# Optimization experiments

Hardware: AMD Instinct MI355X
Metric: run time of the kernel (lower is better)

Reference implementation:

```python
import jax, jax.numpy as jnp
import numpy as np

B, T, D = 512, 512, 256          # batch, timesteps, input feature dim
H0, H1, H2, H3 = 32, 64, 64, 64  # VanillaRNN, LSTM, LSTM, GRU hidden sizes
NC = 12                          # num_cumulants


def setup_inputs() -> dict:
    key = jax.random.key(0)
    ks = jax.random.split(key, 12)
    f32 = jnp.float32

    def w(k, shape, fan_in):
        return jax.random.normal(k, shape, f32) * f32(1.0 / np.sqrt(fan_in))

    inp = {}
    inp["pixels_observation"] = jax.random.normal(ks[0], (B, T, D), f32)
    # VanillaRNN(32): input_to_hidden Linear(D->32), hidden_to_hidden Linear(32->32), both with bias
    inp["van_wi"] = w(ks[1], (D, H0), D)
    inp["van_bi"] = jnp.zeros((H0,), f32)
    inp["van_wh"] = w(ks[2], (H0, H0), H0)
    inp["van_bh"] = jnp.zeros((H0,), f32)
    # LSTM(64) on 32-dim input: Linear(32+64 -> 4*64)
    inp["lstm1_w"] = w(ks[3], (H0 + H1, 4 * H1), H0 + H1)
    inp["lstm1_b"] = jnp.zeros((4 * H1,), f32)
    # LSTM(64) on 64-dim input
    inp["lstm2_w"] = w(ks[4], (H1 + H2, 4 * H2), H1 + H2)
    inp["lstm2_b"] = jnp.zeros((4 * H2,), f32)
    # GRU(64)
    inp["gru_wi"] = w(ks[5], (H2, 3 * H3), H2)
    inp["gru_wh"] = w(ks[6], (H3, 3 * H3), H3)
    inp["gru_b"] = jnp.zeros((3 * H3,), f32)
    # MLP (32, 32, 12)
    inp["mlp_w1"] = w(ks[7], (H3, 32), H3)
    inp["mlp_b1"] = jnp.zeros((32,), f32)
    inp["mlp_w2"] = w(ks[8], (32, 32), 32)
    inp["mlp_b2"] = jnp.zeros((32,), f32)
    inp["mlp_w3"] = w(ks[9], (32, NC), 32)
    inp["mlp_b3"] = jnp.zeros((NC,), f32)
    # learned successor_features parameter (preference_vectors = ones(NC,1) constant)
    inp["successor_features"] = jax.random.normal(ks[10], (NC, 1), f32)
    inp["action_index"] = 0
    return inp


def _lstm_step(x, h, c, w, b):
    # haiku LSTM: gates on concat([x, h]); split order i, g, f, o; forget bias +1
    gated = jnp.concatenate([x, h], axis=-1) @ w + b
    i, g, f, o = jnp.split(gated, 4, axis=-1)
    c = jax.nn.sigmoid(f + 1.0) * c + jax.nn.sigmoid(i) * jnp.tanh(g)
    h = jax.nn.sigmoid(o) * jnp.tanh(c)
    return h, c


def reference(pixels_observation, van_wi, van_bi, van_wh, van_bh,
              lstm1_w, lstm1_b, lstm2_w, lstm2_b,
              gru_wi, gru_wh, gru_b,
              mlp_w1, mlp_b1, mlp_w2, mlp_b2, mlp_w3, mlp_b3,
              successor_features, action_index):
    assert action_index == 0  # source selects branch with a static Python int
    x = pixels_observation
    Bsz = x.shape[0]
    f32 = x.dtype

    def step(carry, x_t):
        h0, h1, c1, h2, c2, h3 = carry
        # VanillaRNN: relu(Wi x + bi + Wh h + bh)
        h0 = jax.nn.relu(x_t @ van_wi + van_bi + h0 @ van_wh + van_bh)
        h1, c1 = _lstm_step(h0, h1, c1, lstm1_w, lstm1_b)
        h2, c2 = _lstm_step(h1, h2, c2, lstm2_w, lstm2_b)
        # haiku GRU
        gates_x = h2 @ gru_wi                       # [B, 3H]
        zr_x, a_x = gates_x[:, :2 * H3], gates_x[:, 2 * H3:]
        zr = zr_x + h3 @ gru_wh[:, :2 * H3] + gru_b[:2 * H3]
        z, r = jnp.split(jax.nn.sigmoid(zr), 2, axis=-1)
        a = jnp.tanh(a_x + (r * h3) @ gru_wh[:, 2 * H3:] + gru_b[2 * H3:])
        h3 = (1.0 - z) * h3 + z * a
        return (h0, h1, c1, h2, c2, h3), None

    init = (jnp.zeros((Bsz, H0), f32),
            jnp.zeros((Bsz, H1), f32), jnp.zeros((Bsz, H1), f32),
            jnp.zeros((Bsz, H2), f32), jnp.zeros((Bsz, H2), f32),
            jnp.zeros((Bsz, H3), f32))
    carry, _ = jax.lax.scan(step, init, jnp.swapaxes(x, 0, 1))  # time-major scan
    emb = carry[-1]  # final GRU output = DeepRNN output at last timestep

    # MLP (32, 32, NC): relu on hidden layers, linear final layer
    emb = jax.nn.relu(emb @ mlp_w1 + mlp_b1)
    emb = jax.nn.relu(emb @ mlp_w2 + mlp_b2)
    emb = emb @ mlp_w3 + mlp_b3                     # [B, NC]

    preference_vectors = jnp.ones((NC, 1), f32)
    # einsum('ca,bc->ba', pref * succ, emb)
    policy_params = emb @ (preference_vectors * successor_features)  # [B, 1]
    return successor_features, preference_vectors, policy_params
```

## Files before the change

kernel.cpp:

```cpp
#include <hip/hip_runtime.h>
#include <stdint.h>

#define Tsz 512
#define Dsz 256
#define NINT 260

union UHp { uint32_t u; _Float16 s[2]; };
__device__ __forceinline__ uint32_t packh(float a, float b) {
    UHp x; x.s[0] = (_Float16)a; x.s[1] = (_Float16)b; return x.u;
}
__device__ __forceinline__ float dot2(uint32_t w, uint32_t a, float c) {
#if __has_builtin(__builtin_amdgcn_fdot2)
    typedef _Float16 h2 __attribute__((ext_vector_type(2)));
    union U { uint32_t u; h2 h; };
    U W, A; W.u = w; A.u = a;
    return __builtin_amdgcn_fdot2(W.h, A.h, c, false);
#else
    float d;
    asm("v_dot2_f32_f16 %0, %1, %2, %3" : "=v"(d) : "v"(w), "v"(a), "v"(c));
    return d;
#endif
}
__device__ __forceinline__ float fsig(float x)  { return 1.0f / (1.0f + __expf(-x)); }
__device__ __forceinline__ float ftanh(float x) { return 2.0f / (1.0f + __expf(-2.0f * x)) - 1.0f; }

__device__ __forceinline__ void barrier_lds() {
    asm volatile("s_waitcnt lgkmcnt(0)" ::: "memory");
    __builtin_amdgcn_s_barrier();
}

#define D4(ACC, WP, V) \
    do { ACC = dot2((WP)[0], (V).x, ACC); ACC = dot2((WP)[1], (V).y, ACC); \
         ACC = dot2((WP)[2], (V).z, ACC); ACC = dot2((WP)[3], (V).w, ACC); } while (0)
#define D4X(A, X, WP, V) \
    do { A = dot2((WP)[0], (V).x, A); X = dot2((WP)[1], (V).y, X); \
         A = dot2((WP)[2], (V).z, A); X = dot2((WP)[3], (V).w, X); } while (0)

__global__ __launch_bounds__(512, 1) void rnn_pipe5(
    const float* __restrict__ pix,
    const float* __restrict__ van_wi, const float* __restrict__ van_bi,
    const float* __restrict__ van_wh, const float* __restrict__ van_bh,
    const float* __restrict__ w1g, const float* __restrict__ b1g,
    const float* __restrict__ w2g, const float* __restrict__ b2g,
    const float* __restrict__ gwi, const float* __restrict__ gwh,
    const float* __restrict__ gb,
    const float* __restrict__ mw1, const float* __restrict__ mb1,
    const float* __restrict__ mw2, const float* __restrict__ mb2,
    const float* __restrict__ mw3, const float* __restrict__ mb3,
    const float* __restrict__ sf,
    float* __restrict__ out)
{
    const int tid  = threadIdx.x;
    const int wv   = tid >> 6;
    const int lane = tid & 63;
    const int r0   = 2 * blockIdx.x;

    __shared__ __align__(16) _Float16 xb [4][2][256];
    __shared__ __align__(16) _Float16 h0b[4][2][32];
    __shared__ __align__(16) _Float16 h1b[4][2][64];
    __shared__ __align__(16) _Float16 h2b[4][2][64];
    __shared__ __align__(16) _Float16 gxb[4][2][192];
    __shared__ __align__(16) _Float16 h3s[2][64];
    __shared__ __align__(16) _Float16 rh3s[2][64];
    __shared__ int flg[4];
    __shared__ float sHf[2][64];
    __shared__ float sT[2][64];
    __shared__ float sP[2][12];

    uint32_t wreg[128];
    float bz0 = 0.f, bz1 = 0.f, bz2 = 0.f;
    float st0 = 0.f, st1 = 0.f;
    float4 pxS[4];
    const float* pr0 = nullptr; const float* pr1 = nullptr;

    if (wv == 0) {
        const int c = lane & 31, s = lane >> 5;
#pragma unroll
        for (int j = 0; j < 64; ++j)
            wreg[j] = packh(van_wi[(128 * s + 2 * j) * 32 + c],
                            van_wi[(128 * s + 2 * j + 1) * 32 + c]);
#pragma unroll
        for (int j = 0; j < 8; ++j)
            wreg[64 + j] = packh(van_wh[(16 * s + 2 * j) * 32 + c],
                                 van_wh[(16 * s + 2 * j + 1) * 32 + c]);
        bz0 = van_bi[c] + van_bh[c];
        pr0 = pix + (size_t)r0 * Tsz * Dsz;
        pr1 = pr0 + (size_t)Tsz * Dsz;
#pragma unroll
        for (int t = 0; t < 2; ++t) {
            float4 p0 = *(const float4*)(pr0 + (size_t)t * Dsz + 4 * lane);
            float4 p1 = *(const float4*)(pr1 + (size_t)t * Dsz + 4 * lane);
            uint32_t* x0 = (uint32_t*)xb[t][0];
            uint32_t* x1 = (uint32_t*)xb[t][1];
            x0[2 * lane] = packh(p0.x, p0.y); x0[2 * lane + 1] = packh(p0.z, p0.w);
            x1[2 * lane] = packh(p1.x, p1.y); x1[2 * lane + 1] = packh(p1.z, p1.w);
        }
        pxS[0] = *(const float4*)(pr0 + 2 * (size_t)Dsz + 4 * lane);
        pxS[1] = *(const float4*)(pr1 + 2 * (size_t)Dsz + 4 * lane);
        pxS[2] = *(const float4*)(pr0 + 3 * (size_t)Dsz + 4 * lane);
        pxS[3] = *(const float4*)(pr1 + 3 * (size_t)Dsz + 4 * lane);
    } else if (wv <= 2) {
        const int p = tid - 64, u = p >> 1, odd = p & 1;
        const int c0 = odd ? 128 + u : u, c1 = c0 + 64;
#pragma unroll
        for (int j = 0; j < 48; ++j)
            wreg[j] = packh(w1g[(2 * j) * 256 + c0], w1g[(2 * j + 1) * 256 + c0]);
#pragma unroll
        for (int j = 0; j < 48; ++j)
            wreg[48 + j] = packh(w1g[(2 * j) * 256 + c1], w1g[(2 * j + 1) * 256 + c1]);
        bz0 = b1g[c0]; bz1 = b1g[c1];
    } else if (wv <= 4) {
        const int p = tid - 192, u = p >> 1, odd = p & 1;
        const int c0 = odd ? 128 + u : u, c1 = c0 + 64;
#pragma unroll
        for (int j = 0; j < 64; ++j)
            wreg[j] = packh(w2g[(2 * j) * 256 + c0], w2g[(2 * j + 1) * 256 + c0]);
#pragma unroll
        for (int j = 0; j < 64; ++j)
            wreg[64 + j] = packh(w2g[(2 * j) * 256 + c1], w2g[(2 * j + 1) * 256 + c1]);
        bz0 = b2g[c0]; bz1 = b2g[c1];
    } else if (wv == 5) {
#pragma unroll
        for (int j = 0; j < 32; ++j) {
            wreg[j]      = packh(gwi[(2 * j) * 192 + lane],       gwi[(2 * j + 1) * 192 + lane]);
            wreg[32 + j] = packh(gwi[(2 * j) * 192 + 64 + lane],  gwi[(2 * j + 1) * 192 + 64 + lane]);
            wreg[64 + j] = packh(gwi[(2 * j) * 192 + 128 + lane], gwi[(2 * j + 1) * 192 + 128 + lane]);
        }
        bz0 = gb[lane]; bz1 = gb[64 + lane]; bz2 = gb[128 + lane];
    } else {
#pragma unroll
        for (int j = 0; j < 32; ++j) {
            wreg[j]      = packh(gwh[(2 * j) * 192 + lane],       gwh[(2 * j + 1) * 192 + lane]);
            wreg[32 + j] = packh(gwh[(2 * j) * 192 + 64 + lane],  gwh[(2 * j + 1) * 192 + 64 + lane]);
            wreg[64 + j] = packh(gwh[(2 * j) * 192 + 128 + lane], gwh[(2 * j + 1) * 192 + 128 + lane]);
        }
    }

    for (int i = tid; i < 4 * 2 * 32;  i += 512) ((_Float16*)h0b)[i] = (_Float16)0.f;
    for (int i = tid; i < 4 * 2 * 64;  i += 512) ((_Float16*)h1b)[i] = (_Float16)0.f;
    for (int i = tid; i < 4 * 2 * 64;  i += 512) ((_Float16*)h2b)[i] = (_Float16)0.f;
    for (int i = tid; i < 4 * 2 * 192; i += 512) ((_Float16*)gxb)[i] = (_Float16)0.f;
    for (int i = tid; i < 2 * 64; i += 512) { ((_Float16*)h3s)[i] = (_Float16)0.f; ((_Float16*)rh3s)[i] = (_Float16)0.f; }
    if (tid < 4) flg[tid] = 0;
    __syncthreads();

    for (int k = 0; k < NINT; ++k) {

        if (wv == 0) {
#pragma unroll
            for (int s = 0; s < 2; ++s) {
                const int t2 = 2 * k + 2 + s;
                if (t2 < Tsz) {
                    uint32_t* x0 = (uint32_t*)xb[t2 & 3][0];
                    uint32_t* x1 = (uint32_t*)xb[t2 & 3][1];
                    float4 a0 = pxS[2 * s], a1 = pxS[2 * s + 1];
                    x0[2 * lane] = packh(a0.x, a0.y); x0[2 * lane + 1] = packh(a0.z, a0.w);
                    x1[2 * lane] = packh(a1.x, a1.y); x1[2 * lane + 1] = packh(a1.z, a1.w);
                }
            }
#pragma unroll
            for (int s = 0; s < 2; ++s) {
                const int t4 = 2 * k + 4 + s;
                if (t4 < Tsz) {
                    pxS[2 * s]     = *(const float4*)(pr0 + (size_t)t4 * Dsz + 4 * lane);
                    pxS[2 * s + 1] = *(const float4*)(pr1 + (size_t)t4 * Dsz + 4 * lane);
                }
            }
            const int c = lane & 31, ssp = lane >> 5;
#pragma unroll
            for (int s = 0; s < 2; ++s) {
                const int t = 2 * k + s;
                if (t < Tsz) {
#pragma unroll
                    for (int r = 0; r < 2; ++r) {
                        const uint4* xq = ((const uint4*)xb[t & 3][r]) + 16 * ssp;
                        const uint4* hq = ((const uint4*)h0b[(t - 1) & 3][r]) + 2 * ssp;
                        float a0 = 0.f, a1 = 0.f;
#pragma unroll
                        for (int q = 0; q < 16; q += 2) {
                            uint4 v0 = xq[q], v1 = xq[q + 1];
                            D4(a0, &wreg[4 * q], v0);
                            D4(a1, &wreg[4 * q + 4], v1);
                        }
                        {
                            uint4 v0 = hq[0], v1 = hq[1];
                            D4(a0, &wreg[64], v0);
                            D4(a1, &wreg[68], v1);
                        }
                        float acc = a0 + a1;
                        acc += __shfl_xor(acc, 32);
                        if (ssp == 0) h0b[t & 3][r][c] = (_Float16)fmaxf(acc + bz0, 0.f);
                    }
                }
            }
        } else if (wv <= 2) {
            const int p = tid - 64, u = p >> 1, odd = p & 1;
#pragma unroll
            for (int s = 0; s < 2; ++s) {
                const int t = 2 * k - 2 + s;
                if (s == 1) {
                    asm volatile("s_waitcnt lgkmcnt(0)" ::: "memory");
                    if (lane == 0) *((volatile int*)&flg[wv - 1]) = k + 1;
                    volatile int* pf = (volatile int*)&flg[(wv - 1) ^ 1];
                    while (*pf < k + 1) {}
                    asm volatile("" ::: "memory");
                }
                if (0 <= t && t < Tsz) {
#pragma unroll
                    for (int r = 0; r < 2; ++r) {
                        const uint4* aq = (const uint4*)h0b[t & 3][r];
                        const uint4* bq = (const uint4*)h1b[(t - 1) & 3][r];
                        float a0 = bz0, a1 = bz1, x0 = 0.f, x1 = 0.f;
#pragma unroll
                        for (int q = 0; q < 4; ++q) {
                            uint4 v = aq[q];
                            D4X(a0, x0, &wreg[4 * q], v);
                            D4X(a1, x1, &wreg[48 + 4 * q], v);
                        }
#pragma unroll
                        for (int q = 0; q < 8; ++q) {
                            uint4 v = bq[q];
                            D4X(a0, x0, &wreg[16 + 4 * q], v);
                            D4X(a1, x1, &wreg[64 + 4 * q], v);
                        }
                        float g0 = a0 + x0, g1 = a1 + x1;
                        float send = 0.f, fq = 0.f, op = 0.f;
                        if (!odd) send = fsig(g0) * ftanh(g1);
                        else { fq = fsig(g0 + 1.f); op = fsig(g1); }
                        float prx = __shfl_xor(send, 1);
                        if (odd) {
                            float cs = r ? st1 : st0;
                            cs = fq * cs + prx;
                            if (r) st1 = cs; else st0 = cs;
                            h1b[t & 3][r][u] = (_Float16)(op * ftanh(cs));
                        }
                    }
                }
            }
        } else if (wv <= 4) {
            const int p = tid - 192, u = p >> 1, odd = p & 1;
#pragma unroll
            for (int s = 0; s < 2; ++s) {
                const int t = 2 * k - 4 + s;
                if (s == 1) {
                    asm volatile("s_waitcnt lgkmcnt(0)" ::: "memory");
                    if (lane == 0) *((volatile int*)&flg[wv - 1]) = k + 1;
                    volatile int* pf = (volatile int*)&flg[(wv - 1) ^ 1];
                    while (*pf < k + 1) {}
                    asm volatile("" ::: "memory");
                }
                if (0 <= t && t < Tsz) {
#pragma unroll
                    for (int r = 0; r < 2; ++r) {
                        const uint4* aq = (const uint4*)h1b[t & 3][r];
                        const uint4* bq = (const uint4*)h2b[(t - 1) & 3][r];
                        float a0 = bz0, a1 = bz1, x0 = 0.f, x1 = 0.f;
#pragma unroll
                        for (int q = 0; q < 8; ++q) {
                            uint4 v = aq[q];
                            D4X(a0, x0, &wreg[4 * q], v);
                            D4X(a1, x1, &wreg[64 + 4 * q], v);
                        }
#pragma unroll
                        for (int q = 0; q < 8; ++q) {
                            uint4 v = bq[q];
                            D4X(a0, x0, &wreg[32 + 4 * q], v);
                            D4X(a1, x1, &wreg[96 + 4 * q], v);
                        }
                        float g0 = a0 + x0, g1 = a1 + x1;
                        float send = 0.f, fq = 0.f, op = 0.f;
                        if (!odd) send = fsig(g0) * ftanh(g1);
                        else { fq = fsig(g0 + 1.f); op = fsig(g1); }
                        float prx = __shfl_xor(send, 1);
                        if (odd) {
                            float cs = r ? st1 : st0;
                            cs = fq * cs + prx;
                            if (r) st1 = cs; else st0 = cs;
                            h2b[t & 3][r][u] = (_Float16)(op * ftanh(cs));
                        }
                    }
                }
            }
        } else if (wv == 5) {
#pragma unroll
            for (int s = 0; s < 2; ++s) {
                const int t = 2 * k - 6 + s;
                if (0 <= t && t < Tsz) {
#pragma unroll
                    for (int r = 0; r < 2; ++r) {
                        const uint4* hq = (const uint4*)h2b[t & 3][r];
                        float az = bz0, ar = bz1, aa = bz2;
#pragma unroll
                        for (int q = 0; q < 8; ++q) {
                            uint4 v = hq[q];
                            D4(az, &wreg[4 * q], v);
                            D4(ar, &wreg[32 + 4 * q], v);
                            D4(aa, &wreg[64 + 4 * q], v);
                        }
                        gxb[t & 3][r][lane]       = (_Float16)az;
                        gxb[t & 3][r][64 + lane]  = (_Float16)ar;
                        gxb[t & 3][r][128 + lane] = (_Float16)aa;
                    }
                }
            }
        } else {
            const int r = wv - 6;
#pragma unroll
            for (int s = 0; s < 2; ++s) {
                const int t = 2 * k - 8 + s;
                if (0 <= t && t < Tsz) {
                    const uint4* hq = (const uint4*)h3s[r];
                    float az = (float)gxb[t & 3][r][lane];
                    float ar = (float)gxb[t & 3][r][64 + lane];
#pragma unroll
                    for (int q = 0; q < 8; ++q) {
                        uint4 v = hq[q];
                        D4(az, &wreg[4 * q], v);
                        D4(ar, &wreg[32 + 4 * q], v);
                    }
                    float z = fsig(az);
                    rh3s[r][lane] = (_Float16)(fsig(ar) * st0);
                    float ga = (float)gxb[t & 3][r][128 + lane];
                    asm volatile("s_waitcnt lgkmcnt(0)" ::: "memory");
                    const uint4* rq = (const uint4*)rh3s[r];
                    float aa = ga, ab = 0.f;
#pragma unroll
                    for (int q = 0; q < 8; ++q) {
                        uint4 v = rq[q];
                        if (q & 1) { D4(ab, &wreg[64 + 4 * q], v); }
                        else       { D4(aa, &wreg[64 + 4 * q], v); }
                    }
                    float av = ftanh(aa + ab);
                    st0 = (1.f - z) * st0 + z * av;
                    h3s[r][lane] = (_Float16)st0;
                }
            }
        }
        barrier_lds();
    }
    __syncthreads();

    if (wv == 6) sHf[0][lane] = st0;
    if (wv == 7) sHf[1][lane] = st0;
    __syncthreads();
    if (tid < 64) {
        const int r = tid >> 5, c = tid & 31;
        float acc = mb1[c];
#pragma unroll
        for (int kk = 0; kk < 64; ++kk) acc = fmaf(sHf[r][kk], mw1[kk * 32 + c], acc);
        sT[r][c] = fmaxf(acc, 0.f);
    }
    __syncthreads();
    if (tid < 64) {
        const int r = tid >> 5, c = tid & 31;
        float acc = mb2[c];
#pragma unroll
        for (int kk = 0; kk < 32; ++kk) acc = fmaf(sT[r][kk], mw2[kk * 32 + c], acc);
        sT[r][32 + c] = fmaxf(acc, 0.f);
    }
    __syncthreads();
    if (tid < 24) {
        const int r = tid / 12, c = tid - 12 * r;
        float acc = mb3[c];
#pragma unroll
        for (int kk = 0; kk < 32; ++kk) acc = fmaf(sT[r][32 + kk], mw3[kk * 12 + c], acc);
        sP[r][c] = acc;
    }
    __syncthreads();
    if (tid < 2) {
        float acc = 0.f;
#pragma unroll
        for (int kk = 0; kk < 12; ++kk) acc = fmaf(sP[tid][kk], sf[kk], acc);
        out[24 + r0 + tid] = acc;
    }
    if (blockIdx.x == 0 && tid < 12) {
        out[tid] = sf[tid];
        out[12 + tid] = 1.0f;
    }
}

extern "C" void kernel_launch(void* const* d_in, const int* in_sizes, int n_in,
                              void* d_out, int out_size, void* d_ws, size_t ws_size,
                              hipStream_t stream) {
    (void)in_sizes; (void)n_in; (void)d_ws; (void)ws_size; (void)out_size;
    const float* pix    = (const float*)d_in[0];
    const float* van_wi = (const float*)d_in[1];
    const float* van_bi = (const float*)d_in[2];
    const float* van_wh = (const float*)d_in[3];
    const float* van_bh = (const float*)d_in[4];
    const float* w1     = (const float*)d_in[5];
    const float* b1     = (const float*)d_in[6];
    const float* w2     = (const float*)d_in[7];
    const float* b2     = (const float*)d_in[8];
    const float* gwi    = (const float*)d_in[9];
    const float* gwh    = (const float*)d_in[10];
    const float* gb     = (const float*)d_in[11];
    const float* mw1    = (const float*)d_in[12];
    const float* mb1    = (const float*)d_in[13];
    const float* mw2    = (const float*)d_in[14];
    const float* mb2    = (const float*)d_in[15];
    const float* mw3    = (const float*)d_in[16];
    const float* mb3    = (const float*)d_in[17];
    const float* sf     = (const float*)d_in[18];
    float* out = (float*)d_out;

    rnn_pipe5<<<256, 512, 0, stream>>>(
        pix, van_wi, van_bi, van_wh, van_bh,
        w1, b1, w2, b2, gwi, gwh, gb,
        mw1, mb1, mw2, mb2, mw3, mb3, sf, out);
}
```

Baseline: 812.6 us.

## Replace lockstep block barriers with per-role LDS progress-flag dataflow sync

Drops the global per-iteration workgroup barrier, which forced all eight wavefronts to advance two timesteps in lockstep. Each wave now polls per-stage progress counters in shared memory and waits only for its producers and for ring-buffer slot reuse. Wave-to-role mapping is also permuted, and the pixel prefetch becomes a simple two-deep register shift. This lets stages drift and overlap freely, at the cost of spin-polling LDS, and correctness now rests on the counter and ordering logic.

```diff
diff --git a/kernel.cpp b/kernel.cpp
--- a/kernel.cpp
+++ b/kernel.cpp
@@ -3,7 +3,15 @@
 
 #define Tsz 512
 #define Dsz 256
-#define NINT 260
+
+#define R_VAN 0
+#define R_L1A 1
+#define R_L1B 2
+#define R_L2A 3
+#define R_L2B 4
+#define R_GX  5
+#define R_GR0 6
+#define R_GR1 7
 
 union UHp { uint32_t u; _Float16 s[2]; };
 __device__ __forceinline__ uint32_t packh(float a, float b) {
@@ -24,11 +32,6 @@
 __device__ __forceinline__ float fsig(float x)  { return 1.0f / (1.0f + __expf(-x)); }
 __device__ __forceinline__ float ftanh(float x) { return 2.0f / (1.0f + __expf(-2.0f * x)) - 1.0f; }
 
-__device__ __forceinline__ void barrier_lds() {
-    asm volatile("s_waitcnt lgkmcnt(0)" ::: "memory");
-    __builtin_amdgcn_s_barrier();
-}
-
 #define D4(ACC, WP, V) \
     do { ACC = dot2((WP)[0], (V).x, ACC); ACC = dot2((WP)[1], (V).y, ACC); \
          ACC = dot2((WP)[2], (V).z, ACC); ACC = dot2((WP)[3], (V).w, ACC); } while (0)
@@ -36,7 +39,18 @@
     do { A = dot2((WP)[0], (V).x, A); X = dot2((WP)[1], (V).y, X); \
          A = dot2((WP)[2], (V).z, A); X = dot2((WP)[3], (V).w, X); } while (0)
 
-__global__ __launch_bounds__(512, 1) void rnn_pipe5(
+#define WAITGE(cache, ridx, need) \
+    do { if ((cache) < (need)) { \
+        volatile const int* _pf = (volatile const int*)&prog[(ridx)]; \
+        int _v = *_pf; \
+        while (_v < (need)) _v = *_pf; \
+        (cache) = _v; } } while (0)
+
+#define SIGNAL(ridx, val) \
+    do { asm volatile("s_waitcnt lgkmcnt(0)" ::: "memory"); \
+         *((volatile int*)&prog[(ridx)]) = (val); } while (0)
+
+__global__ __launch_bounds__(512, 1) void rnn_flag(
     const float* __restrict__ pix,
     const float* __restrict__ van_wi, const float* __restrict__ van_bi,
     const float* __restrict__ van_wh, const float* __restrict__ van_bh,
@@ -55,6 +69,18 @@
     const int lane = tid & 63;
     const int r0   = 2 * blockIdx.x;
 
+    int role;
+    switch (wv) {
+        case 0: role = R_L2A; break;
+        case 1: role = R_L2B; break;
+        case 2: role = R_VAN; break;
+        case 3: role = R_GX;  break;
+        case 4: role = R_GR0; break;
+        case 5: role = R_GR1; break;
+        case 6: role = R_L1A; break;
+        default: role = R_L1B; break;
+    }
+
     __shared__ __align__(16) _Float16 xb [4][2][256];
     __shared__ __align__(16) _Float16 h0b[4][2][32];
     __shared__ __align__(16) _Float16 h1b[4][2][64];
@@ -62,7 +88,7 @@
     __shared__ __align__(16) _Float16 gxb[4][2][192];
     __shared__ __align__(16) _Float16 h3s[2][64];
     __shared__ __align__(16) _Float16 rh3s[2][64];
-    __shared__ int flg[4];
+    __shared__ int prog[8];
     __shared__ float sHf[2][64];
     __shared__ float sT[2][64];
     __shared__ float sP[2][12];
@@ -70,10 +96,10 @@
     uint32_t wreg[128];
     float bz0 = 0.f, bz1 = 0.f, bz2 = 0.f;
     float st0 = 0.f, st1 = 0.f;
-    float4 pxS[4];
+    float4 pxA0{}, pxB0{}, pxA1{}, pxB1{};
     const float* pr0 = nullptr; const float* pr1 = nullptr;
 
-    if (wv == 0) {
+    if (role == R_VAN) {
         const int c = lane & 31, s = lane >> 5;
 #pragma unroll
         for (int j = 0; j < 64; ++j)
@@ -95,12 +121,13 @@
             x0[2 * lane] = packh(p0.x, p0.y); x0[2 * lane + 1] = packh(p0.z, p0.w);
             x1[2 * lane] = packh(p1.x, p1.y); x1[2 * lane + 1] = packh(p1.z, p1.w);
         }
-        pxS[0] = *(const float4*)(pr0 + 2 * (size_t)Dsz + 4 * lane);
-        pxS[1] = *(const float4*)(pr1 + 2 * (size_t)Dsz + 4 * lane);
-        pxS[2] = *(const float4*)(pr0 + 3 * (size_t)Dsz + 4 * lane);
-        pxS[3] = *(const float4*)(pr1 + 3 * (size_t)Dsz + 4 * lane);
-    } else if (wv <= 2) {
-        const int p = tid - 64, u = p >> 1, odd = p & 1;
+        pxA0 = *(const float4*)(pr0 + 2 * (size_t)Dsz + 4 * lane);
+        pxA1 = *(const float4*)(pr1 + 2 * (size_t)Dsz + 4 * lane);
+        pxB0 = *(const float4*)(pr0 + 3 * (size_t)Dsz + 4 * lane);
+        pxB1 = *(const float4*)(pr1 + 3 * (size_t)Dsz + 4 * lane);
+    } else if (role == R_L1A || role == R_L1B) {
+        const int p = (role == R_L1A ? 0 : 64) + lane;
+        const int u = p >> 1, odd = p & 1;
         const int c0 = odd ? 128 + u : u, c1 = c0 + 64;
 #pragma unroll
         for (int j = 0; j < 48; ++j)
@@ -109,8 +136,9 @@
         for (int j = 0; j < 48; ++j)
             wreg[48 + j] = packh(w1g[(2 * j) * 256 + c1], w1g[(2 * j + 1) * 256 + c1]);
         bz0 = b1g[c0]; bz1 = b1g[c1];
-    } else if (wv <= 4) {
-        const int p = tid - 192, u = p >> 1, odd = p & 1;
+    } else if (role == R_L2A || role == R_L2B) {
+        const int p = (role == R_L2A ? 0 : 64) + lane;
+        const int u = p >> 1, odd = p & 1;
         const int c0 = odd ? 128 + u : u, c1 = c0 + 64;
 #pragma unroll
         for (int j = 0; j < 64; ++j)
@@ -119,7 +147,7 @@
         for (int j = 0; j < 64; ++j)
             wreg[64 + j] = packh(w2g[(2 * j) * 256 + c1], w2g[(2 * j + 1) * 256 + c1]);
         bz0 = b2g[c0]; bz1 = b2g[c1];
-    } else if (wv == 5) {
+    } else if (role == R_GX) {
 #pragma unroll
         for (int j = 0; j < 32; ++j) {
             wreg[j]      = packh(gwi[(2 * j) * 192 + lane],       gwi[(2 * j + 1) * 192 + lane]);
@@ -141,208 +169,191 @@
     for (int i = tid; i < 4 * 2 * 64;  i += 512) ((_Float16*)h2b)[i] = (_Float16)0.f;
     for (int i = tid; i < 4 * 2 * 192; i += 512) ((_Float16*)gxb)[i] = (_Float16)0.f;
     for (int i = tid; i < 2 * 64; i += 512) { ((_Float16*)h3s)[i] = (_Float16)0.f; ((_Float16*)rh3s)[i] = (_Float16)0.f; }
-    if (tid < 4) flg[tid] = 0;
+    if (tid < 8) prog[tid] = 0;
     __syncthreads();
 
-    for (int k = 0; k < NINT; ++k) {
-
-        if (wv == 0) {
-#pragma unroll
-            for (int s = 0; s < 2; ++s) {
-                const int t2 = 2 * k + 2 + s;
-                if (t2 < Tsz) {
-                    uint32_t* x0 = (uint32_t*)xb[t2 & 3][0];
-                    uint32_t* x1 = (uint32_t*)xb[t2 & 3][1];
-                    float4 a0 = pxS[2 * s], a1 = pxS[2 * s + 1];
-                    x0[2 * lane] = packh(a0.x, a0.y); x0[2 * lane + 1] = packh(a0.z, a0.w);
-                    x1[2 * lane] = packh(a1.x, a1.y); x1[2 * lane + 1] = packh(a1.z, a1.w);
-                }
-            }
-#pragma unroll
-            for (int s = 0; s < 2; ++s) {
-                const int t4 = 2 * k + 4 + s;
-                if (t4 < Tsz) {
-                    pxS[2 * s]     = *(const float4*)(pr0 + (size_t)t4 * Dsz + 4 * lane);
-                    pxS[2 * s + 1] = *(const float4*)(pr1 + (size_t)t4 * Dsz + 4 * lane);
-                }
-            }
-            const int c = lane & 31, ssp = lane >> 5;
-#pragma unroll
-            for (int s = 0; s < 2; ++s) {
-                const int t = 2 * k + s;
-                if (t < Tsz) {
-#pragma unroll
-                    for (int r = 0; r < 2; ++r) {
-                        const uint4* xq = ((const uint4*)xb[t & 3][r]) + 16 * ssp;
-                        const uint4* hq = ((const uint4*)h0b[(t - 1) & 3][r]) + 2 * ssp;
-                        float a0 = 0.f, a1 = 0.f;
-#pragma unroll
-                        for (int q = 0; q < 16; q += 2) {
-                            uint4 v0 = xq[q], v1 = xq[q + 1];
-                            D4(a0, &wreg[4 * q], v0);
-                            D4(a1, &wreg[4 * q + 4], v1);
-                        }
-                        {
-                            uint4 v0 = hq[0], v1 = hq[1];
-                            D4(a0, &wreg[64], v0);
-                            D4(a1, &wreg[68], v1);
-                        }
-                        float acc = a0 + a1;
-                        acc += __shfl_xor(acc, 32);
-                        if (ssp == 0) h0b[t & 3][r][c] = (_Float16)fmaxf(acc + bz0, 0.f);
-                    }
-                }
-            }
-        } else if (wv <= 2) {
-            const int p = tid - 64, u = p >> 1, odd = p & 1;
-#pragma unroll
-            for (int s = 0; s < 2; ++s) {
-                const int t = 2 * k - 2 + s;
-                if (s == 1) {
-                    asm volatile("s_waitcnt lgkmcnt(0)" ::: "memory");
-                    if (lane == 0) *((volatile int*)&flg[wv - 1]) = k + 1;
-                    volatile int* pf = (volatile int*)&flg[(wv - 1) ^ 1];
-                    while (*pf < k + 1) {}
-                    asm volatile("" ::: "memory");
-                }
-                if (0 <= t && t < Tsz) {
-#pragma unroll
-                    for (int r = 0; r < 2; ++r) {
-                        const uint4* aq = (const uint4*)h0b[t & 3][r];
-                        const uint4* bq = (const uint4*)h1b[(t - 1) & 3][r];
-                        float a0 = bz0, a1 = bz1, x0 = 0.f, x1 = 0.f;
-#pragma unroll
-                        for (int q = 0; q < 4; ++q) {
-                            uint4 v = aq[q];
-                            D4X(a0, x0, &wreg[4 * q], v);
-                            D4X(a1, x1, &wreg[48 + 4 * q], v);
-                        }
-#pragma unroll
-                        for (int q = 0; q < 8; ++q) {
-                            uint4 v = bq[q];
-                            D4X(a0, x0, &wreg[16 + 4 * q], v);
-                            D4X(a1, x1, &wreg[64 + 4 * q], v);
-                        }
-                        float g0 = a0 + x0, g1 = a1 + x1;
-                        float send = 0.f, fq = 0.f, op = 0.f;
-                        if (!odd) send = fsig(g0) * ftanh(g1);
-                        else { fq = fsig(g0 + 1.f); op = fsig(g1); }
-                        float prx = __shfl_xor(send, 1);
-                        if (odd) {
-                            float cs = r ? st1 : st0;
-                            cs = fq * cs + prx;
-                            if (r) st1 = cs; else st0 = cs;
-                            h1b[t & 3][r][u] = (_Float16)(op * ftanh(cs));
-                        }
-                    }
-                }
-            }
-        } else if (wv <= 4) {
-            const int p = tid - 192, u = p >> 1, odd = p & 1;
-#pragma unroll
-            for (int s = 0; s < 2; ++s) {
-                const int t = 2 * k - 4 + s;
-                if (s == 1) {
-                    asm volatile("s_waitcnt lgkmcnt(0)" ::: "memory");
-                    if (lane == 0) *((volatile int*)&flg[wv - 1]) = k + 1;
-                    volatile int* pf = (volatile int*)&flg[(wv - 1) ^ 1];
-                    while (*pf < k + 1) {}
-                    asm volatile("" ::: "memory");
-                }
-                if (0 <= t && t < Tsz) {
-#pragma unroll
-                    for (int r = 0; r < 2; ++r) {
-                        const uint4* aq = (const uint4*)h1b[t & 3][r];
-                        const uint4* bq = (const uint4*)h2b[(t - 1) & 3][r];
-                        float a0 = bz0, a1 = bz1, x0 = 0.f, x1 = 0.f;
-#pragma unroll
-                        for (int q = 0; q < 8; ++q) {
-                            uint4 v = aq[q];
-                            D4X(a0, x0, &wreg[4 * q], v);
-                            D4X(a1, x1, &wreg[64 + 4 * q], v);
-                        }
-#pragma unroll
-                        for (int q = 0; q < 8; ++q) {
-                            uint4 v = bq[q];
-                            D4X(a0, x0, &wreg[32 + 4 * q], v);
-                            D4X(a1, x1, &wreg[96 + 4 * q], v);
-                        }
-                        float g0 = a0 + x0, g1 = a1 + x1;
-                        float send = 0.f, fq = 0.f, op = 0.f;
-                        if (!odd) send = fsig(g0) * ftanh(g1);
-                        else { fq = fsig(g0 + 1.f); op = fsig(g1); }
-                        float prx = __shfl_xor(send, 1);
-                        if (odd) {
-                            float cs = r ? st1 : st0;
-                            cs = fq * cs + prx;
-                            if (r) st1 = cs; else st0 = cs;
-                            h2b[t & 3][r][u] = (_Float16)(op * ftanh(cs));
-                        }
-                    }
-                }
-            }
-        } else if (wv == 5) {
-#pragma unroll
-            for (int s = 0; s < 2; ++s) {
-                const int t = 2 * k - 6 + s;
-                if (0 <= t && t < Tsz) {
-#pragma unroll
-                    for (int r = 0; r < 2; ++r) {
-                        const uint4* hq = (const uint4*)h2b[t & 3][r];
-                        float az = bz0, ar = bz1, aa = bz2;
-#pragma unroll
-                        for (int q = 0; q < 8; ++q) {
-                            uint4 v = hq[q];
-                            D4(az, &wreg[4 * q], v);
-                            D4(ar, &wreg[32 + 4 * q], v);
-                            D4(aa, &wreg[64 + 4 * q], v);
-                        }
-                        gxb[t & 3][r][lane]       = (_Float16)az;
-                        gxb[t & 3][r][64 + lane]  = (_Float16)ar;
-                        gxb[t & 3][r][128 + lane] = (_Float16)aa;
-                    }
-                }
-            }
-        } else {
-            const int r = wv - 6;
-#pragma unroll
-            for (int s = 0; s < 2; ++s) {
-                const int t = 2 * k - 8 + s;
-                if (0 <= t && t < Tsz) {
-                    const uint4* hq = (const uint4*)h3s[r];
-                    float az = (float)gxb[t & 3][r][lane];
-                    float ar = (float)gxb[t & 3][r][64 + lane];
-#pragma unroll
-                    for (int q = 0; q < 8; ++q) {
-                        uint4 v = hq[q];
-                        D4(az, &wreg[4 * q], v);
-                        D4(ar, &wreg[32 + 4 * q], v);
-                    }
-                    float z = fsig(az);
-                    rh3s[r][lane] = (_Float16)(fsig(ar) * st0);
-                    float ga = (float)gxb[t & 3][r][128 + lane];
-                    asm volatile("s_waitcnt lgkmcnt(0)" ::: "memory");
-                    const uint4* rq = (const uint4*)rh3s[r];
-                    float aa = ga, ab = 0.f;
-#pragma unroll
-                    for (int q = 0; q < 8; ++q) {
-                        uint4 v = rq[q];
-                        if (q & 1) { D4(ab, &wreg[64 + 4 * q], v); }
-                        else       { D4(aa, &wreg[64 + 4 * q], v); }
-                    }
-                    float av = ftanh(aa + ab);
-                    st0 = (1.f - z) * st0 + z * av;
-                    h3s[r][lane] = (_Float16)st0;
-                }
-            }
-        }
-        barrier_lds();
-    }
+    if (role == R_VAN) {
+        const int c = lane & 31, s = lane >> 5;
+        int cA = 0, cB = 0;
+        for (int t = 0; t < Tsz; ++t) {
+            WAITGE(cA, R_L1A, t - 3);
+            WAITGE(cB, R_L1B, t - 3);
+            if (t + 2 < Tsz) {
+                uint32_t* x0 = (uint32_t*)xb[(t + 2) & 3][0];
+                uint32_t* x1 = (uint32_t*)xb[(t + 2) & 3][1];
+                x0[2 * lane] = packh(pxA0.x, pxA0.y); x0[2 * lane + 1] = packh(pxA0.z, pxA0.w);
+                x1[2 * lane] = packh(pxA1.x, pxA1.y); x1[2 * lane + 1] = packh(pxA1.z, pxA1.w);
+            }
+            pxA0 = pxB0; pxA1 = pxB1;
+            if (t + 4 < Tsz) {
+                pxB0 = *(const float4*)(pr0 + (size_t)(t + 4) * Dsz + 4 * lane);
+                pxB1 = *(const float4*)(pr1 + (size_t)(t + 4) * Dsz + 4 * lane);
+            }
+#pragma unroll
+            for (int r = 0; r < 2; ++r) {
+                const uint4* xq = ((const uint4*)xb[t & 3][r]) + 16 * s;
+                const uint4* hq = ((const uint4*)h0b[(t - 1) & 3][r]) + 2 * s;
+                float a0 = 0.f, a1 = 0.f;
+#pragma unroll
+                for (int q = 0; q < 16; q += 2) {
+                    uint4 v0 = xq[q], v1 = xq[q + 1];
+                    D4(a0, &wreg[4 * q], v0);
+                    D4(a1, &wreg[4 * q + 4], v1);
+                }
+                {
+                    uint4 v0 = hq[0], v1 = hq[1];
+                    D4(a0, &wreg[64], v0);
+                    D4(a1, &wreg[68], v1);
+                }
+                float acc = a0 + a1;
+                acc += __shfl_xor(acc, 32);
+                if (s == 0) h0b[t & 3][r][c] = (_Float16)fmaxf(acc + bz0, 0.f);
+            }
+            SIGNAL(R_VAN, t + 1);
+        }
+    } else if (role == R_L1A || role == R_L1B) {
+        const int prt = (role == R_L1A) ? R_L1B : R_L1A;
+        const int p = (role == R_L1A ? 0 : 64) + lane;
+        const int u = p >> 1, odd = p & 1;
+        int cv = 0, cp = 0, c2a = 0, c2b = 0;
+        for (int t = 0; t < Tsz; ++t) {
+            WAITGE(cv, R_VAN, t + 1);
+            WAITGE(cp, prt, t);
+            WAITGE(c2a, R_L2A, t - 3);
+            WAITGE(c2b, R_L2B, t - 3);
+#pragma unroll
+            for (int r = 0; r < 2; ++r) {
+                const uint4* aq = (const uint4*)h0b[t & 3][r];
+                const uint4* bq = (const uint4*)h1b[(t - 1) & 3][r];
+                float a0 = bz0, a1 = bz1, x0 = 0.f, x1 = 0.f;
+#pragma unroll
+                for (int q = 0; q < 4; ++q) {
+                    uint4 v = aq[q];
+                    D4X(a0, x0, &wreg[4 * q], v);
+                    D4X(a1, x1, &wreg[48 + 4 * q], v);
+                }
+#pragma unroll
+                for (int q = 0; q < 8; ++q) {
+                    uint4 v = bq[q];
+                    D4X(a0, x0, &wreg[16 + 4 * q], v);
+                    D4X(a1, x1, &wreg[64 + 4 * q], v);
+                }
+                float g0 = a0 + x0, g1 = a1 + x1;
+                float send = 0.f, fq = 0.f, op = 0.f;
+                if (!odd) send = fsig(g0) * ftanh(g1);
+                else { fq = fsig(g0 + 1.f); op = fsig(g1); }
+                float prx = __shfl_xor(send, 1);
+                if (odd) {
+                    float cs = r ? st1 : st0;
+                    cs = fq * cs + prx;
+                    if (r) st1 = cs; else st0 = cs;
+                    h1b[t & 3][r][u] = (_Float16)(op * ftanh(cs));
+                }
+            }
+            SIGNAL(role, t + 1);
+        }
+    } else if (role == R_L2A || role == R_L2B) {
+        const int prt = (role == R_L2A) ? R_L2B : R_L2A;
+        const int p = (role == R_L2A ? 0 : 64) + lane;
+        const int u = p >> 1, odd = p & 1;
+        int c1a = 0, c1b = 0, cp = 0, cg = 0;
+        for (int t = 0; t < Tsz; ++t) {
+            WAITGE(c1a, R_L1A, t + 1);
+            WAITGE(c1b, R_L1B, t + 1);
+            WAITGE(cp, prt, t);
+            WAITGE(cg, R_GX, t - 3);
+#pragma unroll
+            for (int r = 0; r < 2; ++r) {
+                const uint4* aq = (const uint4*)h1b[t & 3][r];
+                const uint4* bq = (const uint4*)h2b[(t - 1) & 3][r];
+                float a0 = bz0, a1 = bz1, x0 = 0.f, x1 = 0.f;
+#pragma unroll
+                for (int q = 0; q < 8; ++q) {
+                    uint4 v = aq[q];
+                    D4X(a0, x0, &wreg[4 * q], v);
+                    D4X(a1, x1, &wreg[64 + 4 * q], v);
+                }
+#pragma unroll
+                for (int q = 0; q < 8; ++q) {
+                    uint4 v = bq[q];
+                    D4X(a0, x0, &wreg[32 + 4 * q], v);
+                    D4X(a1, x1, &wreg[96 + 4 * q], v);
+                }
+                float g0 = a0 + x0, g1 = a1 + x1;
+                float send = 0.f, fq = 0.f, op = 0.f;
+                if (!odd) send = fsig(g0) * ftanh(g1);
+                else { fq = fsig(g0 + 1.f); op = fsig(g1); }
+                float prx = __shfl_xor(send, 1);
+                if (odd) {
+                    float cs = r ? st1 : st0;
+                    cs = fq * cs + prx;
+                    if (r) st1 = cs; else st0 = cs;
+                    h2b[t & 3][r][u] = (_Float16)(op * ftanh(cs));
+                }
+            }
+            SIGNAL(role, t + 1);
+        }
+    } else if (role == R_GX) {
+        int c2a = 0, c2b = 0, g0c = 0, g1c = 0;
+        for (int t = 0; t < Tsz; ++t) {
+            WAITGE(c2a, R_L2A, t + 1);
+            WAITGE(c2b, R_L2B, t + 1);
+            WAITGE(g0c, R_GR0, t - 3);
+            WAITGE(g1c, R_GR1, t - 3);
+#pragma unroll
+            for (int r = 0; r < 2; ++r) {
+                const uint4* hq = (const uint4*)h2b[t & 3][r];
+                float az = bz0, ar = bz1, aa = bz2;
+#pragma unroll
+                for (int q = 0; q < 8; ++q) {
+                    uint4 v = hq[q];
+                    D4(az, &wreg[4 * q], v);
+                    D4(ar, &wreg[32 + 4 * q], v);
+                    D4(aa, &wreg[64 + 4 * q], v);
+                }
+                gxb[t & 3][r][lane]       = (_Float16)az;
+                gxb[t & 3][r][64 + lane]  = (_Float16)ar;
+                gxb[t & 3][r][128 + lane] = (_Float16)aa;
+            }
+            SIGNAL(R_GX, t + 1);
+        }
+    } else {
+        const int r = (role == R_GR0) ? 0 : 1;
+        int cg = 0;
+        for (int t = 0; t < Tsz; ++t) {
+            WAITGE(cg, R_GX, t + 1);
+            const uint4* hq = (const uint4*)h3s[r];
+            float az = (float)gxb[t & 3][r][lane];
+            float ar = (float)gxb[t & 3][r][64 + lane];
+#pragma unroll
+            for (int q = 0; q < 8; ++q) {
+                uint4 v = hq[q];
+                D4(az, &wreg[4 * q], v);
+                D4(ar, &wreg[32 + 4 * q], v);
+            }
+            float z = fsig(az);
+            rh3s[r][lane] = (_Float16)(fsig(ar) * st0);
+            float ga = (float)gxb[t & 3][r][128 + lane];
+            asm volatile("s_waitcnt lgkmcnt(0)" ::: "memory");
+            const uint4* rq = (const uint4*)rh3s[r];
+            float aa = ga, ab = 0.f;
+#pragma unroll
+            for (int q = 0; q < 8; ++q) {
+                uint4 v = rq[q];
+                if (q & 1) { D4(ab, &wreg[64 + 4 * q], v); }
+                else       { D4(aa, &wreg[64 + 4 * q], v); }
+            }
+            float av = ftanh(aa + ab);
+            st0 = (1.f - z) * st0 + z * av;
+            h3s[r][lane] = (_Float16)st0;
+            SIGNAL(role, t + 1);
+        }
+    }
+
+    if (role == R_GR0) sHf[0][lane] = st0;
+    if (role == R_GR1) sHf[1][lane] = st0;
     __syncthreads();
 
-    if (wv == 6) sHf[0][lane] = st0;
-    if (wv == 7) sHf[1][lane] = st0;
-    __syncthreads();
     if (tid < 64) {
         const int r = tid >> 5, c = tid & 31;
         float acc = mb1[c];
@@ -404,7 +415,7 @@
     const float* sf     = (const float*)d_in[18];
     float* out = (float*)d_out;
 
-    rnn_pipe5<<<256, 512, 0, stream>>>(
+    rnn_flag<<<256, 512, 0, stream>>>(
         pix, van_wi, van_bi, van_wh, van_bh,
         w1, b1, w2, b2, gwi, gwh, gb,
         mw1, mb1, mw2, mb2, mw3, mb3, sf, out);
```

Result: faster. 781.1 us (-3.9%).
